# Kernel optimization log

Measured on AMD Instinct MI355X. Metric: run time of the kernel, lower is better.

The kernel has to match this reference:

```python
import jax, jax.numpy as jnp
import numpy as np

N, A, G, C = 16, 4096, 256, 80
ALPHA, GAMMA, CLS_LAMBDA = 0.25, 2.0, 1.0
BIG = 1e8


def setup_inputs() -> dict:
    key = jax.random.key(0)
    k1, k2, k3, k4, k5, k6 = jax.random.split(key, 6)
    return {
        "gt_padded": jax.random.uniform(k1, (N, G, 4), dtype=jnp.float32),
        "prop_boxes": jax.random.uniform(k2, (N, A, 4), dtype=jnp.float32),
        "pred_boxes": jax.random.uniform(k3, (N, A, 4), dtype=jnp.float32),
        "class_logits": jax.random.normal(k4, (N, A, C), dtype=jnp.float32),
        "gt_masks": jax.random.randint(k5, (N, G), 0, 2).astype(bool),
        "gt_classes": jax.random.randint(k6, (N, G), 0, C),
    }


def _box_distances(b1, b2):
    # b1: [N, A, 4], b2: [N, G, 4] -> pairwise L1 distance [N, A, G]
    return jnp.abs(b1[:, :, None, :] - b2[:, None, :, :]).sum(-1)


def _sigmoid_focal_loss(logits, one_hot, alpha, gamma):
    p = jax.nn.sigmoid(logits)
    # stable BCE-with-logits
    ce = jnp.maximum(logits, 0.0) - logits * one_hot + jnp.log1p(jnp.exp(-jnp.abs(logits)))
    p_t = p * one_hot + (1.0 - p) * (1.0 - one_hot)
    loss = ce * (1.0 - p_t) ** gamma
    alpha_t = alpha * one_hot + (1.0 - alpha) * (1.0 - one_hot)
    return alpha_t * loss


def reference(gt_padded, prop_boxes, pred_boxes, class_logits, gt_masks, gt_classes):
    mask_row = gt_masks[:, None, :]  # [N, 1, G]

    # proposal -> gt pairwise L1, masked argmin over gt axis
    prop_d = jnp.where(mask_row, _box_distances(prop_boxes, gt_padded), BIG)
    closest = jnp.argmin(prop_d, axis=-1)  # [N, A]

    # projection loss: pred -> gt distance gathered at proposals' closest gt
    pred_d = jnp.where(mask_row, _box_distances(pred_boxes, gt_padded), BIG)
    proj = jnp.take_along_axis(pred_d, closest[..., None], axis=2)[..., 0]  # [N, A]
    mask_gathered = jnp.take_along_axis(gt_masks, closest, axis=1)  # [N, A]
    projection_loss = jnp.where(mask_gathered, proj, 0.0)

    # classification target: class of closest gt (0 when image has no gt)
    nonempty = gt_masks.any(-1)  # [N]
    target = jnp.take_along_axis(gt_classes, closest, axis=1)  # [N, A]
    target = jnp.where(nonempty[:, None], target, 0)

    one_hot = jax.nn.one_hot(target, C, dtype=class_logits.dtype)
    cls = _sigmoid_focal_loss(class_logits, one_hot, ALPHA, GAMMA).mean(-1)  # [N, A]
    classification_loss = jnp.where(nonempty[:, None], cls, 0.0) * CLS_LAMBDA

    return classification_loss, projection_loss
```

## Files before the change

### kernel.cpp

```cpp
#include <hip/hip_runtime.h>

#define N_ 16
#define A_ 4096
#define G_ 256
#define C_ 80
#define BIG_ 1e8f
#define LN2_ 0.69314718055994531f


#define DPP_XOR1  0xB1
#define DPP_XOR2  0x4E
#define DPP_XOR7  0x141
#define DPP_XOR15 0x140

template<int CTRL>
__device__ __forceinline__ float dppf(float x) {
    return __int_as_float(__builtin_amdgcn_update_dpp(
        0, __float_as_int(x), CTRL, 0xF, 0xF, true));
}
template<int CTRL>
__device__ __forceinline__ int dppi(int x) {
    return __builtin_amdgcn_update_dpp(0, x, CTRL, 0xF, 0xF, true);
}

template<int CTRL>
__device__ __forceinline__ void argmin_stage(float& d, int& idx) {
    const float od = dppf<CTRL>(d);
    const int   oc = dppi<CTRL>(idx);
    const bool  bt = (od < d) || (od == d && oc < idx);
    d   = bt ? od : d;
    idx = bt ? oc : idx;
}

__global__ __launch_bounds__(256, 4) void cbppl_fused_kernel(
    const float* __restrict__ gt_padded,
    const float* __restrict__ prop_boxes,
    const float* __restrict__ pred_boxes,
    const float* __restrict__ class_logits,
    const int*   __restrict__ gt_masks,
    const int*   __restrict__ gt_classes,
    float* __restrict__ out_cls,
    float* __restrict__ out_proj)
{
    __shared__ float4 s_gt[G_];
    __shared__ int    s_cls[G_];

    const int t   = threadIdx.x;
    const int sub = t & 15;
    const int n   = blockIdx.x >> 6;
    const int ab  = (blockIdx.x & 63) << 6;

    {
        const int gidx = n * G_ + t;
        float4 g4 = ((const float4*)gt_padded)[gidx];
        if (!gt_masks[gidx]) { g4.x = BIG_; g4.y = BIG_; g4.z = BIG_; g4.w = BIG_; }
        s_gt[t]  = g4;
        s_cls[t] = gt_classes[gidx];
    }
    __syncthreads();

    float4 b[16];
    #pragma unroll
    for (int m = 0; m < 16; ++m) b[m] = s_gt[sub + (m << 4)];

    for (int p = 0; p < 4; ++p) {
        const int ai  = ((t >> 6) << 4) + (p << 2) + ((t >> 4) & 3);
        const int row = n * A_ + ab + ai;

        const float4 pb = ((const float4*)prop_boxes)[row];
        const float4 qb = ((const float4*)pred_boxes)[row];

        const float* lrow = class_logits + (size_t)row * C_;
        float xv[5];
        #pragma unroll
        for (int k = 0; k < 5; ++k) xv[k] = lrow[sub + (k << 4)];

        float dloc = INFINITY;
        int   mloc = 0;
        #pragma unroll
        for (int m = 0; m < 16; ++m) {
            const float d = fabsf(pb.x - b[m].x) + fabsf(pb.y - b[m].y)
                          + fabsf(pb.z - b[m].z) + fabsf(pb.w - b[m].w);
            if (d < dloc) { dloc = d; mloc = m; }
        }
        int iloc = (mloc << 4) + sub;

        argmin_stage<DPP_XOR1 >(dloc, iloc);
        argmin_stage<DPP_XOR2 >(dloc, iloc);
        argmin_stage<DPP_XOR7 >(dloc, iloc);
        argmin_stage<DPP_XOR15>(dloc, iloc);
        const int   closest  = iloc;
        const int   nonempty = (dloc < BIG_);

        const float4 cb     = s_gt[closest];
        const int    target = s_cls[closest];
        const float  pd = fabsf(qb.x - cb.x) + fabsf(qb.y - cb.y)
                        + fabsf(qb.z - cb.z) + fabsf(qb.w - cb.w);

        float acc = 0.0f;
        #pragma unroll
        for (int j = 0; j < 5; ++j) {
            const float x  = xv[j];
            const float u  = __expf(-x);
            const float tt = 1.0f + u;
            const float sp = fmaf(LN2_, __log2f(tt), x);
            const float r  = __builtin_amdgcn_rcpf(tt);
            acc = fmaf(sp, r * r, acc);
        }
        acc *= 0.75f;

        {
            const int kt = target >> 4;
            float xt = xv[0];
            xt = (kt == 1) ? xv[1] : xt;
            xt = (kt == 2) ? xv[2] : xt;
            xt = (kt == 3) ? xv[3] : xt;
            xt = (kt == 4) ? xv[4] : xt;
            const float u  = __expf(-xt);
            const float tt = 1.0f + u;
            const float sp = fmaf(LN2_, __log2f(tt), xt);
            const float pp = __builtin_amdgcn_rcpf(tt);
            const float q  = 1.0f - pp;
            const float corr = fmaf(0.25f * (sp - xt), q * q,
                                    -0.75f * sp * pp * pp);
            acc += ((target & 15) == sub) ? corr : 0.0f;
        }

        acc += dppf<DPP_XOR1 >(acc);
        acc += dppf<DPP_XOR2 >(acc);
        acc += dppf<DPP_XOR7 >(acc);
        acc += dppf<DPP_XOR15>(acc);

        if (sub == 0) {
            out_cls[row]  = nonempty ? acc * (1.0f / (float)C_) : 0.0f;
            out_proj[row] = nonempty ? pd : 0.0f;
        }
    }
}

extern "C" void kernel_launch(void* const* d_in, const int* in_sizes, int n_in,
                              void* d_out, int out_size, void* d_ws, size_t ws_size,
                              hipStream_t stream) {
    const float* gt_padded    = (const float*)d_in[0];
    const float* prop_boxes   = (const float*)d_in[1];
    const float* pred_boxes   = (const float*)d_in[2];
    const float* class_logits = (const float*)d_in[3];
    const int*   gt_masks     = (const int*)d_in[4];
    const int*   gt_classes   = (const int*)d_in[5];

    float* out = (float*)d_out;
    float* out_cls  = out;
    float* out_proj = out + N_ * A_;

    dim3 grid(N_ * A_ / 64);
    dim3 block(256);
    cbppl_fused_kernel<<<grid, block, 0, stream>>>(
        gt_padded, prop_boxes, pred_boxes, class_logits,
        gt_masks, gt_classes, out_cls, out_proj);
}
```

Before: 14.84 us.

## Pack argmin distance, gt index and class into a 64-bit min key

```diff
diff --git a/kernel.cpp b/kernel.cpp
--- a/kernel.cpp
+++ b/kernel.cpp
@@ -14,23 +14,22 @@
 #define DPP_XOR15 0x140
 
 template<int CTRL>
-__device__ __forceinline__ float dppf(float x) {
-    return __int_as_float(__builtin_amdgcn_update_dpp(
-        0, __float_as_int(x), CTRL, 0xF, 0xF, true));
-}
-template<int CTRL>
 __device__ __forceinline__ int dppi(int x) {
     return __builtin_amdgcn_update_dpp(0, x, CTRL, 0xF, 0xF, true);
 }
+template<int CTRL>
+__device__ __forceinline__ float dppf(float x) {
+    return __int_as_float(dppi<CTRL>(__float_as_int(x)));
+}
+template<int CTRL>
+__device__ __forceinline__ void kmin_stage(unsigned long long& key) {
+    const unsigned lo = (unsigned)dppi<CTRL>((int)(unsigned)key);
+    const unsigned hi = (unsigned)dppi<CTRL>((int)(unsigned)(key >> 32));
+    const unsigned long long o = ((unsigned long long)hi << 32) | lo;
+    key = (o < key) ? o : key;
+}
 
-template<int CTRL>
-__device__ __forceinline__ void argmin_stage(float& d, int& idx) {
-    const float od = dppf<CTRL>(d);
-    const int   oc = dppi<CTRL>(idx);
-    const bool  bt = (od < d) || (od == d && oc < idx);
-    d   = bt ? od : d;
-    idx = bt ? oc : idx;
-}
+typedef float f4a4 __attribute__((ext_vector_type(4), aligned(4)));
 
 __global__ __launch_bounds__(256, 4) void cbppl_fused_kernel(
     const float* __restrict__ gt_padded,
@@ -43,7 +42,7 @@
     float* __restrict__ out_proj)
 {
     __shared__ float4 s_gt[G_];
-    __shared__ int    s_cls[G_];
+    __shared__ int    s_meta[G_];
 
     const int t   = threadIdx.x;
     const int sub = t & 15;
@@ -54,14 +53,18 @@
         const int gidx = n * G_ + t;
         float4 g4 = ((const float4*)gt_padded)[gidx];
         if (!gt_masks[gidx]) { g4.x = BIG_; g4.y = BIG_; g4.z = BIG_; g4.w = BIG_; }
-        s_gt[t]  = g4;
-        s_cls[t] = gt_classes[gidx];
+        s_gt[t]   = g4;
+        s_meta[t] = (t << 8) | gt_classes[gidx];
     }
     __syncthreads();
 
     float4 b[16];
+    int    meta[16];
     #pragma unroll
-    for (int m = 0; m < 16; ++m) b[m] = s_gt[sub + (m << 4)];
+    for (int m = 0; m < 16; ++m) {
+        b[m]    = s_gt[sub + (m << 4)];
+        meta[m] = s_meta[sub + (m << 4)];
+    }
 
     for (int p = 0; p < 4; ++p) {
         const int ai  = ((t >> 6) << 4) + (p << 2) + ((t >> 4) & 3);
@@ -70,37 +73,38 @@
         const float4 pb = ((const float4*)prop_boxes)[row];
         const float4 qb = ((const float4*)pred_boxes)[row];
 
-        const float* lrow = class_logits + (size_t)row * C_;
-        float xv[5];
-        #pragma unroll
-        for (int k = 0; k < 5; ++k) xv[k] = lrow[sub + (k << 4)];
+        const float* lrow = class_logits + (size_t)row * C_ + sub * 5;
+        const f4a4  x4  = *(const f4a4*)lrow;
+        const float x4v = lrow[4];
 
         float dloc = INFINITY;
-        int   mloc = 0;
+        int   mt   = 0;
         #pragma unroll
         for (int m = 0; m < 16; ++m) {
             const float d = fabsf(pb.x - b[m].x) + fabsf(pb.y - b[m].y)
                           + fabsf(pb.z - b[m].z) + fabsf(pb.w - b[m].w);
-            if (d < dloc) { dloc = d; mloc = m; }
+            if (d < dloc) { dloc = d; mt = meta[m]; }
         }
-        int iloc = (mloc << 4) + sub;
 
-        argmin_stage<DPP_XOR1 >(dloc, iloc);
-        argmin_stage<DPP_XOR2 >(dloc, iloc);
-        argmin_stage<DPP_XOR7 >(dloc, iloc);
-        argmin_stage<DPP_XOR15>(dloc, iloc);
-        const int   closest  = iloc;
-        const int   nonempty = (dloc < BIG_);
+        unsigned long long key =
+            ((unsigned long long)__float_as_uint(dloc) << 32) | (unsigned)mt;
+        kmin_stage<DPP_XOR1 >(key);
+        kmin_stage<DPP_XOR2 >(key);
+        kmin_stage<DPP_XOR7 >(key);
+        kmin_stage<DPP_XOR15>(key);
 
-        const float4 cb     = s_gt[closest];
-        const int    target = s_cls[closest];
-        const float  pd = fabsf(qb.x - cb.x) + fabsf(qb.y - cb.y)
-                        + fabsf(qb.z - cb.z) + fabsf(qb.w - cb.w);
+        const int   target   = (int)(key & 0xFF);
+        const int   closest  = (int)((key >> 8) & 0xFF);
+        const float dmin     = __uint_as_float((unsigned)(key >> 32));
+        const int   nonempty = (dmin < BIG_);
 
+        const float4 cb = s_gt[closest];
+
+        const float xs[5] = {x4.x, x4.y, x4.z, x4.w, x4v};
         float acc = 0.0f;
         #pragma unroll
         for (int j = 0; j < 5; ++j) {
-            const float x  = xv[j];
+            const float x  = xs[j];
             const float u  = __expf(-x);
             const float tt = 1.0f + u;
             const float sp = fmaf(LN2_, __log2f(tt), x);
@@ -110,12 +114,12 @@
         acc *= 0.75f;
 
         {
-            const int kt = target >> 4;
-            float xt = xv[0];
-            xt = (kt == 1) ? xv[1] : xt;
-            xt = (kt == 2) ? xv[2] : xt;
-            xt = (kt == 3) ? xv[3] : xt;
-            xt = (kt == 4) ? xv[4] : xt;
+            const int rel = target - sub * 5;
+            float xt = xs[0];
+            xt = (rel == 1) ? xs[1] : xt;
+            xt = (rel == 2) ? xs[2] : xt;
+            xt = (rel == 3) ? xs[3] : xt;
+            xt = (rel == 4) ? xs[4] : xt;
             const float u  = __expf(-xt);
             const float tt = 1.0f + u;
             const float sp = fmaf(LN2_, __log2f(tt), xt);
@@ -123,13 +127,16 @@
             const float q  = 1.0f - pp;
             const float corr = fmaf(0.25f * (sp - xt), q * q,
                                     -0.75f * sp * pp * pp);
-            acc += ((target & 15) == sub) ? corr : 0.0f;
+            acc += ((unsigned)rel < 5u) ? corr : 0.0f;
         }
 
         acc += dppf<DPP_XOR1 >(acc);
         acc += dppf<DPP_XOR2 >(acc);
         acc += dppf<DPP_XOR7 >(acc);
         acc += dppf<DPP_XOR15>(acc);
+
+        const float pd = fabsf(qb.x - cb.x) + fabsf(qb.y - cb.y)
+                       + fabsf(qb.z - cb.z) + fabsf(qb.w - cb.w);
 
         if (sub == 0) {
             out_cls[row]  = nonempty ? acc * (1.0f / (float)C_) : 0.0f;
```

After: 15.75 us. +6.1%, slower.
